# Optimization experiments

Hardware: AMD Instinct MI355X
Metric: run time of the kernel (lower is better)

The kernel has to match this reference:

```python
import jax, jax.numpy as jnp
import numpy as np

B, IN, OUT = 128, 1024, 1024
HILL_N, HILL_KA = 2.0, 0.5  # Hill(n=2, k_a=0.5)


def setup_inputs() -> dict:
    key = jax.random.key(0)
    k0, k1, k2, k3 = jax.random.split(key, 4)
    bound = 1.0 / np.sqrt(IN)  # torch Linear default init range
    inputs = jax.random.normal(k0, (B, IN), dtype=jnp.float32)
    W_nmda = jax.random.uniform(k1, (OUT, IN), jnp.float32, -bound, bound)
    W_non = jax.random.uniform(k2, (OUT, IN), jnp.float32, -bound, bound)
    b_non = jax.random.uniform(k3, (OUT,), jnp.float32, -bound, bound)
    return {"inputs": inputs, "W_nmda": W_nmda, "W_non": W_non, "b_non": b_non}


def reference(inputs, W_nmda, W_non, b_non):
    # state = sigmoid(non_nmda(x)) - 1   in (-1, 0)
    state = jax.nn.sigmoid(inputs @ W_non.T + b_non) - 1.0  # [B, OUT]
    # per-synapse outer product: [B, OUT, IN]
    syn = inputs[:, None, :] * W_nmda[None, :, :]
    # conv1d with fixed filter [0.5, 0.5], stride 1, no padding, then sum over width
    cluster = 0.5 * (syn[..., :-1] + syn[..., 1:])  # [B, OUT, IN-1]
    cluster_activity = jax.nn.relu(cluster.sum(-1))  # [B, OUT]
    # Hill cooperativity with state-modulated coefficient
    n_modif = HILL_N + state
    k_d = HILL_KA ** n_modif
    xn = cluster_activity ** n_modif
    y = xn / (k_d + xn)
    return y + state
```

## Files before the change

kernel.cpp:

```cpp
#include <hip/hip_runtime.h>

#define IN_  1024
#define OUT_ 1024

typedef _Float16 f16x8 __attribute__((ext_vector_type(8)));
typedef float    f32x4 __attribute__((ext_vector_type(4)));

__global__ __launch_bounds__(512, 1) void dendritic_fused(
    const float* __restrict__ x,
    const float* __restrict__ Wn,
    const float* __restrict__ Wo,
    const float* __restrict__ bo,
    float* __restrict__ out) {
  __shared__ __align__(16) char lds[65536];

  const int tid = threadIdx.x;
  const int w   = tid >> 6;
  const int l   = tid & 63;
  const int g   = blockIdx.x & 63;
  const int mq  = blockIdx.x >> 6;
  const int m0  = mq * 32;
  const int n0  = g * 16;

  const int c8 = tid & 31;
  const int rb = tid >> 5;
  const int swz = (rb & 7) << 4;
  const float* srcrow[4];
  srcrow[0] = x  + (size_t)(m0 + rb)      * IN_ + c8 * 8;
  srcrow[1] = x  + (size_t)(m0 + 16 + rb) * IN_ + c8 * 8;
  srcrow[2] = Wn + (size_t)(n0 + rb)      * IN_ + c8 * 8;
  srcrow[3] = Wo + (size_t)(n0 + rb)      * IN_ + c8 * 8;
  int dstoff[4];
  dstoff[0] = rb * 512                + ((c8 * 16) ^ swz);
  dstoff[1] = (16 + rb) * 512         + ((c8 * 16) ^ swz);
  dstoff[2] = 16384 + rb * 512        + ((c8 * 16) ^ swz);
  dstoff[3] = 16384 + 8192 + rb * 512 + ((c8 * 16) ^ swz);

  float4 v[4][2];

#define LOAD(ch)                                                         \
  _Pragma("unroll")                                                      \
  for (int i = 0; i < 4; ++i) {                                          \
    const float4* p = (const float4*)(srcrow[i] + (ch) * 256);           \
    v[i][0] = p[0];                                                      \
    v[i][1] = p[1];                                                      \
  }

#define WRITE(ch)                                                        \
  _Pragma("unroll")                                                      \
  for (int i = 0; i < 4; ++i) {                                          \
    f16x8 h = { (_Float16)v[i][0].x, (_Float16)v[i][0].y,                \
                (_Float16)v[i][0].z, (_Float16)v[i][0].w,                \
                (_Float16)v[i][1].x, (_Float16)v[i][1].y,                \
                (_Float16)v[i][1].z, (_Float16)v[i][1].w };              \
    if (i == 2) {       \
      if ((ch) == 0 && c8 == 0)  h[0] = h[0] * (_Float16)0.5f;           \
      if ((ch) == 3 && c8 == 31) h[7] = h[7] * (_Float16)0.5f;           \
    }                                                                    \
    *(f16x8*)(lds + dstoff[i]) = h;                                      \
  }

  const int fr = l & 15;
  const int cb = ((w * 64 + (l >> 4) * 16) ^ ((fr & 7) << 4));
  const char* pa0 = lds + fr * 512 + cb;
  const char* pa1 = lds + (16 + fr) * 512 + cb;
  const char* pbn = lds + 16384 + fr * 512 + cb;
  const char* pbw = lds + 16384 + 8192 + fr * 512 + cb;

  f32x4 acc00 = {0.f,0.f,0.f,0.f}, acc01 = {0.f,0.f,0.f,0.f};
  f32x4 acc10 = {0.f,0.f,0.f,0.f}, acc11 = {0.f,0.f,0.f,0.f};

  LOAD(0);
  WRITE(0);
  LOAD(1);
  __syncthreads();
#pragma unroll
  for (int c = 0; c < 4; ++c) {
    f16x8 a0 = *(const f16x8*)pa0;
    f16x8 a1 = *(const f16x8*)pa1;
    f16x8 bn = *(const f16x8*)pbn;
    f16x8 bw = *(const f16x8*)pbw;
    acc00 = __builtin_amdgcn_mfma_f32_16x16x32_f16(a0, bn, acc00, 0, 0, 0);
    acc01 = __builtin_amdgcn_mfma_f32_16x16x32_f16(a0, bw, acc01, 0, 0, 0);
    acc10 = __builtin_amdgcn_mfma_f32_16x16x32_f16(a1, bn, acc10, 0, 0, 0);
    acc11 = __builtin_amdgcn_mfma_f32_16x16x32_f16(a1, bw, acc11, 0, 0, 0);
    __syncthreads();
    if (c < 3) {
      WRITE(c + 1);
      if (c < 2) LOAD(c + 2);
      __syncthreads();
    }
  }

  *(f32x4*)(lds + 32768 + (((w * 2 + 0) * 2 + 0) * 64 + l) * 16) = acc00;
  *(f32x4*)(lds + 32768 + (((w * 2 + 0) * 2 + 1) * 64 + l) * 16) = acc01;
  *(f32x4*)(lds + 32768 + (((w * 2 + 1) * 2 + 0) * 64 + l) * 16) = acc10;
  *(f32x4*)(lds + 32768 + (((w * 2 + 1) * 2 + 1) * 64 + l) * 16) = acc11;
  __syncthreads();

  if (tid < 128) {
    const int mt = tid >> 6;
    const int ll = tid & 63;
    f32x4 sN = {0.f,0.f,0.f,0.f}, sO = {0.f,0.f,0.f,0.f};
#pragma unroll
    for (int q = 0; q < 8; ++q) {
      sN += *(const f32x4*)(lds + 32768 + (((q * 2 + mt) * 2 + 0) * 64 + ll) * 16);
      sO += *(const f32x4*)(lds + 32768 + (((q * 2 + mt) * 2 + 1) * 64 + ll) * 16);
    }
    const int n = n0 + (ll & 15);
    const float bias = bo[n];
#pragma unroll
    for (int r = 0; r < 4; ++r) {
      const int m = m0 + mt * 16 + (ll >> 4) * 4 + r;
      const float zN = sN[r];
      const float zO = sO[r] + bias;
      const float state = 1.f / (1.f + expf(-zO)) - 1.f;
      const float nm    = 2.f + state;
      const float kd    = exp2f(-nm);
      const float ca    = fmaxf(zN, 0.f);
      const float xn    = (ca > 0.f) ? exp2f(nm * log2f(ca)) : 0.f;
      out[(size_t)m * OUT_ + n] = xn / (kd + xn) + state;
    }
  }
#undef LOAD
#undef WRITE
}

extern "C" void kernel_launch(void* const* d_in, const int* in_sizes, int n_in,
                              void* d_out, int out_size, void* d_ws, size_t ws_size,
                              hipStream_t stream) {
  const float* x  = (const float*)d_in[0];
  const float* Wn = (const float*)d_in[1];
  const float* Wo = (const float*)d_in[2];
  const float* bo = (const float*)d_in[3];
  float* out = (float*)d_out;
  dendritic_fused<<<dim3(256), dim3(512), 0, stream>>>(x, Wn, Wo, bo, out);
}
```

Baseline: 10.49 us.

## Prefetch all four K-chunks upfront and double-buffer LDS to halve barriers

All global loads for the four K chunks are issued at kernel start into registers, so memory latency is paid once rather than serialised across chunk iterations. LDS is split into two 32KB buffers that alternate, which drops one __syncthreads per chunk. The final reduction scratch moves to offset 0, reusing buffer A after the last barrier. This raises register pressure (32 float4 live), which the 512-thread, single-block launch bound can absorb.

```diff
diff --git a/kernel.cpp b/kernel.cpp
--- a/kernel.cpp
+++ b/kernel.cpp
@@ -22,80 +22,90 @@
   const int m0  = mq * 32;
   const int n0  = g * 16;
 
-  const int c8 = tid & 31;
-  const int rb = tid >> 5;
+  const int c8  = tid & 31;
+  const int rb  = tid >> 5;
   const int swz = (rb & 7) << 4;
-  const float* srcrow[4];
-  srcrow[0] = x  + (size_t)(m0 + rb)      * IN_ + c8 * 8;
-  srcrow[1] = x  + (size_t)(m0 + 16 + rb) * IN_ + c8 * 8;
-  srcrow[2] = Wn + (size_t)(n0 + rb)      * IN_ + c8 * 8;
-  srcrow[3] = Wo + (size_t)(n0 + rb)      * IN_ + c8 * 8;
-  int dstoff[4];
-  dstoff[0] = rb * 512                + ((c8 * 16) ^ swz);
-  dstoff[1] = (16 + rb) * 512         + ((c8 * 16) ^ swz);
-  dstoff[2] = 16384 + rb * 512        + ((c8 * 16) ^ swz);
-  dstoff[3] = 16384 + 8192 + rb * 512 + ((c8 * 16) ^ swz);
+  const float* srcrow0 = x  + (size_t)(m0 + rb)      * IN_ + c8 * 8;
+  const float* srcrow1 = x  + (size_t)(m0 + 16 + rb) * IN_ + c8 * 8;
+  const float* srcrow2 = Wn + (size_t)(n0 + rb)      * IN_ + c8 * 8;
+  const float* srcrow3 = Wo + (size_t)(n0 + rb)      * IN_ + c8 * 8;
+  const int d0 = rb * 512                + ((c8 * 16) ^ swz);
+  const int d1 = (16 + rb) * 512         + ((c8 * 16) ^ swz);
+  const int d2 = 16384 + rb * 512        + ((c8 * 16) ^ swz);
+  const int d3 = 16384 + 8192 + rb * 512 + ((c8 * 16) ^ swz);
 
-  float4 v[4][2];
+  float4 v0[4][2], v1[4][2], v2[4][2], v3[4][2];
 
-#define LOAD(ch)                                                         \
-  _Pragma("unroll")                                                      \
-  for (int i = 0; i < 4; ++i) {                                          \
-    const float4* p = (const float4*)(srcrow[i] + (ch) * 256);           \
-    v[i][0] = p[0];                                                      \
-    v[i][1] = p[1];                                                      \
-  }
+#define LOADC(vv, ch) do {                                                \
+    const float4* p0 = (const float4*)(srcrow0 + (ch) * 256);             \
+    const float4* p1 = (const float4*)(srcrow1 + (ch) * 256);             \
+    const float4* p2 = (const float4*)(srcrow2 + (ch) * 256);             \
+    const float4* p3 = (const float4*)(srcrow3 + (ch) * 256);             \
+    vv[0][0] = p0[0]; vv[0][1] = p0[1];                                   \
+    vv[1][0] = p1[0]; vv[1][1] = p1[1];                                   \
+    vv[2][0] = p2[0]; vv[2][1] = p2[1];                                   \
+    vv[3][0] = p3[0]; vv[3][1] = p3[1];                                   \
+  } while (0)
 
-#define WRITE(ch)                                                        \
-  _Pragma("unroll")                                                      \
-  for (int i = 0; i < 4; ++i) {                                          \
-    f16x8 h = { (_Float16)v[i][0].x, (_Float16)v[i][0].y,                \
-                (_Float16)v[i][0].z, (_Float16)v[i][0].w,                \
-                (_Float16)v[i][1].x, (_Float16)v[i][1].y,                \
-                (_Float16)v[i][1].z, (_Float16)v[i][1].w };              \
-    if (i == 2) {       \
-      if ((ch) == 0 && c8 == 0)  h[0] = h[0] * (_Float16)0.5f;           \
-      if ((ch) == 3 && c8 == 31) h[7] = h[7] * (_Float16)0.5f;           \
-    }                                                                    \
-    *(f16x8*)(lds + dstoff[i]) = h;                                      \
-  }
+#define WRITEC(vv, ch, bb) do {                                           \
+    _Pragma("unroll")                                                     \
+    for (int i = 0; i < 4; ++i) {                                         \
+      f16x8 h = { (_Float16)vv[i][0].x, (_Float16)vv[i][0].y,             \
+                  (_Float16)vv[i][0].z, (_Float16)vv[i][0].w,             \
+                  (_Float16)vv[i][1].x, (_Float16)vv[i][1].y,             \
+                  (_Float16)vv[i][1].z, (_Float16)vv[i][1].w };           \
+      if (i == 2) {       \
+        if ((ch) == 0 && c8 == 0)  h[0] = h[0] * (_Float16)0.5f;          \
+        if ((ch) == 3 && c8 == 31) h[7] = h[7] * (_Float16)0.5f;          \
+      }                                                                   \
+      const int dd = (i == 0 ? d0 : i == 1 ? d1 : i == 2 ? d2 : d3);      \
+      *(f16x8*)(lds + (bb) + dd) = h;                                     \
+    }                                                                     \
+  } while (0)
 
   const int fr = l & 15;
   const int cb = ((w * 64 + (l >> 4) * 16) ^ ((fr & 7) << 4));
-  const char* pa0 = lds + fr * 512 + cb;
-  const char* pa1 = lds + (16 + fr) * 512 + cb;
-  const char* pbn = lds + 16384 + fr * 512 + cb;
-  const char* pbw = lds + 16384 + 8192 + fr * 512 + cb;
+  const int o_a0 = fr * 512 + cb;
+  const int o_a1 = (16 + fr) * 512 + cb;
+  const int o_bn = 16384 + fr * 512 + cb;
+  const int o_bw = 16384 + 8192 + fr * 512 + cb;
 
   f32x4 acc00 = {0.f,0.f,0.f,0.f}, acc01 = {0.f,0.f,0.f,0.f};
   f32x4 acc10 = {0.f,0.f,0.f,0.f}, acc11 = {0.f,0.f,0.f,0.f};
 
-  LOAD(0);
-  WRITE(0);
-  LOAD(1);
+#define COMPUTE(bb) do {                                                  \
+    f16x8 a0 = *(const f16x8*)(lds + (bb) + o_a0);                        \
+    f16x8 a1 = *(const f16x8*)(lds + (bb) + o_a1);                        \
+    f16x8 bn = *(const f16x8*)(lds + (bb) + o_bn);                        \
+    f16x8 bw = *(const f16x8*)(lds + (bb) + o_bw);                        \
+    acc00 = __builtin_amdgcn_mfma_f32_16x16x32_f16(a0, bn, acc00, 0,0,0); \
+    acc01 = __builtin_amdgcn_mfma_f32_16x16x32_f16(a0, bw, acc01, 0,0,0); \
+    acc10 = __builtin_amdgcn_mfma_f32_16x16x32_f16(a1, bn, acc10, 0,0,0); \
+    acc11 = __builtin_amdgcn_mfma_f32_16x16x32_f16(a1, bw, acc11, 0,0,0); \
+  } while (0)
+
+  LOADC(v0, 0);
+  LOADC(v1, 1);
+  LOADC(v2, 2);
+  LOADC(v3, 3);
+
+  WRITEC(v0, 0, 0);
   __syncthreads();
-#pragma unroll
-  for (int c = 0; c < 4; ++c) {
-    f16x8 a0 = *(const f16x8*)pa0;
-    f16x8 a1 = *(const f16x8*)pa1;
-    f16x8 bn = *(const f16x8*)pbn;
-    f16x8 bw = *(const f16x8*)pbw;
-    acc00 = __builtin_amdgcn_mfma_f32_16x16x32_f16(a0, bn, acc00, 0, 0, 0);
-    acc01 = __builtin_amdgcn_mfma_f32_16x16x32_f16(a0, bw, acc01, 0, 0, 0);
-    acc10 = __builtin_amdgcn_mfma_f32_16x16x32_f16(a1, bn, acc10, 0, 0, 0);
-    acc11 = __builtin_amdgcn_mfma_f32_16x16x32_f16(a1, bw, acc11, 0, 0, 0);
-    __syncthreads();
-    if (c < 3) {
-      WRITE(c + 1);
-      if (c < 2) LOAD(c + 2);
-      __syncthreads();
-    }
-  }
+  COMPUTE(0);
+  WRITEC(v1, 1, 32768);
+  __syncthreads();
+  COMPUTE(32768);
+  WRITEC(v2, 2, 0);
+  __syncthreads();
+  COMPUTE(0);
+  WRITEC(v3, 3, 32768);
+  __syncthreads();
+  COMPUTE(32768);
 
-  *(f32x4*)(lds + 32768 + (((w * 2 + 0) * 2 + 0) * 64 + l) * 16) = acc00;
-  *(f32x4*)(lds + 32768 + (((w * 2 + 0) * 2 + 1) * 64 + l) * 16) = acc01;
-  *(f32x4*)(lds + 32768 + (((w * 2 + 1) * 2 + 0) * 64 + l) * 16) = acc10;
-  *(f32x4*)(lds + 32768 + (((w * 2 + 1) * 2 + 1) * 64 + l) * 16) = acc11;
+  *(f32x4*)(lds + (((w * 2 + 0) * 2 + 0) * 64 + l) * 16) = acc00;
+  *(f32x4*)(lds + (((w * 2 + 0) * 2 + 1) * 64 + l) * 16) = acc01;
+  *(f32x4*)(lds + (((w * 2 + 1) * 2 + 0) * 64 + l) * 16) = acc10;
+  *(f32x4*)(lds + (((w * 2 + 1) * 2 + 1) * 64 + l) * 16) = acc11;
   __syncthreads();
 
   if (tid < 128) {
@@ -104,8 +114,8 @@
     f32x4 sN = {0.f,0.f,0.f,0.f}, sO = {0.f,0.f,0.f,0.f};
 #pragma unroll
     for (int q = 0; q < 8; ++q) {
-      sN += *(const f32x4*)(lds + 32768 + (((q * 2 + mt) * 2 + 0) * 64 + ll) * 16);
-      sO += *(const f32x4*)(lds + 32768 + (((q * 2 + mt) * 2 + 1) * 64 + ll) * 16);
+      sN += *(const f32x4*)(lds + (((q * 2 + mt) * 2 + 0) * 64 + ll) * 16);
+      sO += *(const f32x4*)(lds + (((q * 2 + mt) * 2 + 1) * 64 + ll) * 16);
     }
     const int n = n0 + (ll & 15);
     const float bias = bo[n];
@@ -122,8 +132,9 @@
       out[(size_t)m * OUT_ + n] = xn / (kd + xn) + state;
     }
   }
-#undef LOAD
-#undef WRITE
+#undef LOADC
+#undef WRITEC
+#undef COMPUTE
 }
 
 extern "C" void kernel_launch(void* const* d_in, const int* in_sizes, int n_in,
```

New measurement: 10.61 us. About the same (+1.1%).
